# Optimization experiments

Hardware: AMD Instinct MI355X
Metric: run time of the kernel (lower is better)

Reference implementation:

```python
import math
import jax, jax.numpy as jnp
import numpy as np

B, N, M, C, H, POS = 2, 2048, 64, 256, 8, 6
D = C // H  # head_dim = 32
SCALE = 1.0 / math.sqrt(D)
LAMDA = 1.0


def setup_inputs() -> dict:
    key = jax.random.key(0)
    ks = jax.random.split(key, 15)
    s = 0.05
    return {
        "pairwise_g": jax.random.normal(ks[0], (B, N, N, POS), jnp.float32),
        "coset_functions": jax.random.normal(ks[1], (B, N, C), jnp.float32),
        "mask": jnp.ones((B, N), dtype=bool),
        "Wq": jax.random.normal(ks[2], (C, C), jnp.float32) * s,
        "bq": jax.random.normal(ks[3], (C,), jnp.float32) * s,
        "Wk": jax.random.normal(ks[4], (C, C), jnp.float32) * s,
        "bk": jax.random.normal(ks[5], (C,), jnp.float32) * s,
        "Wl": jax.random.normal(ks[6], (C, POS), jnp.float32) * s,
        "bl": jax.random.normal(ks[7], (C,), jnp.float32) * s,
        "u": jax.random.normal(ks[8], (H, D), jnp.float32) * s,
        "v": jax.random.normal(ks[9], (H, D), jnp.float32) * s,
        "Wi": jax.random.normal(ks[10], (C, C), jnp.float32) * s,
        "bi": jax.random.normal(ks[11], (C,), jnp.float32) * s,
        "Wo": jax.random.normal(ks[12], (C, C), jnp.float32) * s,
        "bo": jax.random.normal(ks[13], (C,), jnp.float32) * s,
    }


def reference(pairwise_g, coset_functions, mask, Wq, bq, Wk, bk, Wl, bl, u, v, Wi, bi, Wo, bo):
    # ---- extract_neighbourhoods (mc_samples=M, fill=1.0 -> k == k_ball, permutation irrelevant)
    dists = jnp.linalg.norm(pairwise_g, axis=-1)                      # (B,N,N)
    dists = jnp.where(mask[:, None, :], dists, jnp.float32(1e8))
    _, nbhd_idx = jax.lax.top_k(-dists, M)                            # (B,N,M) nearest neighbors
    nbhd_pg = jnp.take_along_axis(pairwise_g, nbhd_idx[..., None], axis=2)  # (B,N,M,POS)
    gather_rows = jax.vmap(lambda arr, ix: arr[ix])                   # gather along point axis per batch
    nbhd_cf = gather_rows(coset_functions, nbhd_idx)                  # (B,N,M,C)
    nbhd_mask = gather_rows(mask, nbhd_idx)                           # (B,N,M)

    # ---- RelativePositionKernel
    Q = (coset_functions @ Wq.T + bq).reshape(B, N, H, D).transpose(0, 2, 1, 3)  # (B,H,N,D)
    K = (coset_functions @ Wk.T + bk).reshape(B, N, H, D).transpose(0, 2, 1, 3)  # (B,H,N,D)
    e = (nbhd_pg @ Wl.T + bl).reshape(B, N, M, H, D)                  # (B,N,M,H,D)

    S = jnp.einsum('bhnd,bhkd->bhnk', Q, K)                           # dense scores (as original)
    Sg = jnp.take_along_axis(S, nbhd_idx[:, None, :, :], axis=3)      # (B,H,N,M)
    e_term = jnp.einsum('bnmhd,bhnd->bhnm', e, Q + v[None, :, None, :])
    uK = jnp.einsum('hd,bhkd->bhk', u, K)                             # (B,H,N)
    uKg = jnp.take_along_axis(uK[:, :, None, :], nbhd_idx[:, None, :, :], axis=3)  # (B,H,N,M)
    A = (Sg + LAMDA * e_term + uKg) * SCALE
    A = A.transpose(0, 2, 3, 1)                                       # (B,N,M,H)

    # ---- masked softmax over neighbors
    A = jnp.where(nbhd_mask[..., None], A, jnp.float32(-1e38))
    attn = jax.nn.softmax(A, axis=2)                                  # (B,N,M,H)

    # ---- value projection + weighted sum + output linear
    Vv = (nbhd_cf @ Wi.T + bi).reshape(B, N, M, H, D)                 # (B,N,M,H,D)
    out = jnp.einsum('bnmh,bnmhd->bnhd', attn, Vv).reshape(B, N, C)
    out = out @ Wo.T + bo                                             # (B,N,c_out)
    return out
```

## Files before the change

### kernel.cpp

```cpp
#include <hip/hip_runtime.h>
#include <stdint.h>

#define NB 2
#define NN 2048
#define MM 64
#define CC 256
#define HH 8
#define DD 32
#define PP 6
#define ATT_SCALE 0.17677669529663687f

typedef __attribute__((ext_vector_type(8))) short short8;
typedef __attribute__((ext_vector_type(4))) float f32x4;

__device__ __forceinline__ uint16_t f2bf(float f) {
  union { float f; uint32_t u; } c; c.f = f;
  return (uint16_t)((c.u + 0x7fffu + ((c.u >> 16) & 1u)) >> 16);
}

__global__ __launch_bounds__(256) void k_cvt(const float* __restrict__ cf,
                                             const float* __restrict__ Wq,
                                             const float* __restrict__ Wk,
                                             const float* __restrict__ Wi,
                                             const float* __restrict__ Wo,
                                             uint16_t* __restrict__ dst) {
  const int g = blockIdx.x * 256 + threadIdx.x;
  const float* src; int off;
  if (g < 262144)      { src = cf; off = g; }
  else if (g < 278528) { src = Wq; off = g - 262144; }
  else if (g < 294912) { src = Wk; off = g - 278528; }
  else if (g < 311296) { src = Wi; off = g - 294912; }
  else                 { src = Wo; off = g - 311296; }
  const float4 v4 = *(const float4*)(src + (size_t)off * 4);
  ushort4 o;
  o.x = f2bf(v4.x); o.y = f2bf(v4.y); o.z = f2bf(v4.z); o.w = f2bf(v4.w);
  *(ushort4*)(dst + (size_t)g * 4) = o;
}

__global__ __launch_bounds__(256) void k_select(const float* __restrict__ pg,
                                                int* __restrict__ nidx) {
  const int row = blockIdx.x;
  const int t = threadIdx.x;

  __shared__ float s_red[256];
  __shared__ float s_red2[256];
  __shared__ uint32_t s_hist[256];
  __shared__ uint32_t s_scan[256];
  __shared__ float s_cd[NN];
  __shared__ int   s_cj[NN];
  __shared__ int s_tbin;
  __shared__ uint32_t s_c0;
  __shared__ int s_cw;
  __shared__ int s_ct;

  if (t < MM) nidx[(size_t)row * MM + t] = t;

  const float2* base = (const float2*)(pg + (size_t)row * NN * PP);

  float d[8];
  float mn = 3.4e38f, mx = -3.4e38f;
#pragma unroll
  for (int i = 0; i < 8; i++) {
    const int j = t + i * 256;
    const float2 p0 = base[(size_t)j * 3 + 0];
    const float2 p1 = base[(size_t)j * 3 + 1];
    const float2 p2 = base[(size_t)j * 3 + 2];
    float s = __fmul_rn(p0.x, p0.x);
    s = __fadd_rn(s, __fmul_rn(p0.y, p0.y));
    s = __fadd_rn(s, __fmul_rn(p1.x, p1.x));
    s = __fadd_rn(s, __fmul_rn(p1.y, p1.y));
    s = __fadd_rn(s, __fmul_rn(p2.x, p2.x));
    s = __fadd_rn(s, __fmul_rn(p2.y, p2.y));
    const float dist = __fsqrt_rn(s);
    d[i] = dist;
    mn = fminf(mn, dist);
    mx = fmaxf(mx, dist);
  }

  s_red[t] = mn; s_red2[t] = mx;
  __syncthreads();
  for (int off = 128; off; off >>= 1) {
    if (t < off) {
      s_red[t] = fminf(s_red[t], s_red[t + off]);
      s_red2[t] = fmaxf(s_red2[t], s_red2[t + off]);
    }
    __syncthreads();
  }
  mn = s_red[0];
  mx = s_red2[0];
  const float range = mx - mn;
  const float scale = (range > 0.f) ? (256.0f / range) : 0.f;

  s_hist[t] = 0;
  __syncthreads();
  int bins[8];
#pragma unroll
  for (int i = 0; i < 8; i++) {
    int bn = (int)((d[i] - mn) * scale);
    bn = (bn > 255) ? 255 : (bn < 0 ? 0 : bn);
    bins[i] = bn;
    atomicAdd(&s_hist[bn], 1u);
  }
  __syncthreads();

  s_scan[t] = s_hist[t];
  __syncthreads();
  for (int off = 1; off < 256; off <<= 1) {
    const uint32_t add = (t >= off) ? s_scan[t - off] : 0u;
    __syncthreads();
    s_scan[t] += add;
    __syncthreads();
  }

  if (t == 0) { s_cw = 0; s_ct = 0; }
  if (s_scan[t] >= (uint32_t)MM && (t == 0 || s_scan[t - 1] < (uint32_t)MM)) {
    s_tbin = t;
    s_c0 = (t == 0) ? 0u : s_scan[t - 1];
  }
  __syncthreads();

  const int tbin = s_tbin;
  const int c0 = (int)s_c0;

#pragma unroll
  for (int i = 0; i < 8; i++) {
    const int j = t + i * 256;
    if (bins[i] < tbin) {
      const int pos = atomicAdd(&s_cw, 1);
      if (pos < MM) nidx[(size_t)row * MM + pos] = j;
    } else if (bins[i] == tbin) {
      const int pos = atomicAdd(&s_ct, 1);
      s_cd[pos] = d[i];
      s_cj[pos] = j;
    }
  }
  __syncthreads();

  if (t < 64) {
    const int cnt = s_ct;
    const int r = MM - c0;
    for (int it = 0; it < r; ++it) {
      float bd = 3.4e38f; int bj = 0x7fffffff; int bi = -1;
      for (int i = t; i < cnt; i += 64) {
        const float dd = s_cd[i]; const int jj = s_cj[i];
        if (dd < bd || (dd == bd && jj < bj)) { bd = dd; bj = jj; bi = i; }
      }
#pragma unroll
      for (int off = 32; off; off >>= 1) {
        const float od = __shfl_xor(bd, off);
        const int oj = __shfl_xor(bj, off);
        const int oi = __shfl_xor(bi, off);
        if (od < bd || (od == bd && oj < bj)) { bd = od; bj = oj; bi = oi; }
      }
      if (t == 0 && bi >= 0) {
        s_cd[bi] = 3.4e38f;
        nidx[(size_t)row * MM + c0 + it] = bj;
      }
      __threadfence_block();
    }
  }
}

__device__ __forceinline__ void gemm_bt_body(const uint16_t* __restrict__ A,
                                             const uint16_t* __restrict__ W,
                                             const float* __restrict__ bias,
                                             float* __restrict__ O) {
  const int wave = threadIdx.x >> 6;
  const int lane = threadIdx.x & 63;
  const int m = lane & 15;
  const int quad = lane >> 4;
  const int row0 = blockIdx.x * 64 + wave * 16;
  const int c0 = blockIdx.y * 64;

  f32x4 acc0 = {0.f, 0.f, 0.f, 0.f};
  f32x4 acc1 = {0.f, 0.f, 0.f, 0.f};
  f32x4 acc2 = {0.f, 0.f, 0.f, 0.f};
  f32x4 acc3 = {0.f, 0.f, 0.f, 0.f};

#pragma unroll
  for (int k0 = 0; k0 < CC; k0 += 32) {
    const short8 a = *(const short8*)(A + (size_t)(row0 + m) * CC + k0 + quad * 8);
    const short8 b0 = *(const short8*)(W + (size_t)(c0 + 0 + m) * CC + k0 + quad * 8);
    const short8 b1 = *(const short8*)(W + (size_t)(c0 + 16 + m) * CC + k0 + quad * 8);
    const short8 b2 = *(const short8*)(W + (size_t)(c0 + 32 + m) * CC + k0 + quad * 8);
    const short8 b3 = *(const short8*)(W + (size_t)(c0 + 48 + m) * CC + k0 + quad * 8);
    acc0 = __builtin_amdgcn_mfma_f32_16x16x32_bf16(a, b0, acc0, 0, 0, 0);
    acc1 = __builtin_amdgcn_mfma_f32_16x16x32_bf16(a, b1, acc1, 0, 0, 0);
    acc2 = __builtin_amdgcn_mfma_f32_16x16x32_bf16(a, b2, acc2, 0, 0, 0);
    acc3 = __builtin_amdgcn_mfma_f32_16x16x32_bf16(a, b3, acc3, 0, 0, 0);
  }

  const int orow = row0 + quad * 4;
  f32x4 accs[4] = {acc0, acc1, acc2, acc3};
#pragma unroll
  for (int f = 0; f < 4; ++f) {
    const int col = c0 + f * 16 + m;
    const float bv = bias[col];
#pragma unroll
    for (int r = 0; r < 4; ++r) {
      O[(size_t)(orow + r) * CC + col] = accs[f][r] + bv;
    }
  }
}

__global__ __launch_bounds__(256) void k_gemm_qkv(
    const uint16_t* __restrict__ A,
    const uint16_t* __restrict__ W0, const uint16_t* __restrict__ W1, const uint16_t* __restrict__ W2,
    const float* __restrict__ b0, const float* __restrict__ b1, const float* __restrict__ b2,
    float* __restrict__ O0, float* __restrict__ O1, float* __restrict__ O2) {
  const uint16_t* W = (blockIdx.z == 0) ? W0 : ((blockIdx.z == 1) ? W1 : W2);
  const float* bias = (blockIdx.z == 0) ? b0 : ((blockIdx.z == 1) ? b1 : b2);
  float* O = (blockIdx.z == 0) ? O0 : ((blockIdx.z == 1) ? O1 : O2);
  gemm_bt_body(A, W, bias, O);
}

__global__ __launch_bounds__(256) void k_gemm_out(const uint16_t* __restrict__ A,
                                                  const uint16_t* __restrict__ W,
                                                  const float* __restrict__ bias,
                                                  float* __restrict__ O) {
  gemm_bt_body(A, W, bias, O);
}

__global__ __launch_bounds__(256) void k_attn(const float* __restrict__ pg,
                                              const int* __restrict__ nidx,
                                              const float* __restrict__ Q,
                                              const float* __restrict__ K,
                                              const float* __restrict__ V,
                                              const float* __restrict__ Wl,
                                              const float* __restrict__ bl,
                                              const float* __restrict__ u,
                                              const float* __restrict__ v,
                                              uint16_t* __restrict__ attnV) {
  const int row = blockIdx.x;
  const int b = row >> 11;
  const int t = threadIdx.x;
  const int wave = t >> 6;
  const int lane = t & 63;

  __shared__ int s_idx[MM];
  __shared__ float s_npg[MM][7];
  __shared__ float s_qu[CC];
  __shared__ float s_wt[HH][8];
  __shared__ float s_sc[HH][MM];

  if (t < MM) s_idx[t] = nidx[(size_t)row * MM + t] & (NN - 1);
  const float qv_ = Q[(size_t)row * CC + t];
  s_qu[t] = qv_ + u[t];
  __syncthreads();

  if (t < MM) {
    const int jj = s_idx[t];
    const float2* p = (const float2*)(pg + ((size_t)row * NN + (size_t)jj) * PP);
    const float2 p0 = p[0], p1 = p[1], p2 = p[2];
    s_npg[t][0] = p0.x; s_npg[t][1] = p0.y;
    s_npg[t][2] = p1.x; s_npg[t][3] = p1.y;
    s_npg[t][4] = p2.x; s_npg[t][5] = p2.y;
  }

  {
    const int h = t >> 5;
    const float qpv = qv_ + v[t];
    float part[7];
#pragma unroll
    for (int p = 0; p < 6; p++) part[p] = Wl[(size_t)t * PP + p] * qpv;
    part[6] = bl[t] * qpv;
#pragma unroll
    for (int off = 1; off < 32; off <<= 1) {
#pragma unroll
      for (int p = 0; p < 7; p++) part[p] += __shfl_xor(part[p], off);
    }
    if ((t & 31) == 0) {
#pragma unroll
      for (int p = 0; p < 7; p++) s_wt[h][p] = part[p];
    }
  }
  __syncthreads();

#pragma unroll
  for (int pr = 0; pr < 2; ++pr) {
    const int h = wave + pr * 4;
    const int m = lane;
    const int kidx = s_idx[m];
    const float* krow = K + ((size_t)(b * NN + kidx)) * CC + h * DD;
    float acc = s_wt[h][6];
#pragma unroll
    for (int p = 0; p < 6; p++) acc += s_npg[m][p] * s_wt[h][p];
    const float* qu = &s_qu[h * DD];
    float a2 = 0.f;
#pragma unroll
    for (int dd = 0; dd < DD; dd += 4) {
      const float4 kv = *(const float4*)(krow + dd);
      a2 += qu[dd] * kv.x + qu[dd + 1] * kv.y + qu[dd + 2] * kv.z + qu[dd + 3] * kv.w;
    }
    s_sc[h][m] = (acc + a2) * ATT_SCALE;
  }
  __syncthreads();

#pragma unroll
  for (int pr = 0; pr < 2; ++pr) {
    const int h = wave + pr * 4;
    const float x = s_sc[h][lane];
    float mxv = x;
#pragma unroll
    for (int off = 32; off; off >>= 1) mxv = fmaxf(mxv, __shfl_xor(mxv, off));
    const float e = expf(x - mxv);
    float sm = e;
#pragma unroll
    for (int off = 32; off; off >>= 1) sm += __shfl_xor(sm, off);
    s_sc[h][lane] = e / sm;
  }
  __syncthreads();

  {
    const int h = t >> 5;
    const float* Vb = V + (size_t)b * NN * CC;
    float acc = 0.f;
#pragma unroll 4
    for (int m = 0; m < MM; m++) {
      acc += s_sc[h][m] * Vb[(size_t)s_idx[m] * CC + t];
    }
    attnV[(size_t)row * CC + t] = f2bf(acc);
  }
}

extern "C" void kernel_launch(void* const* d_in, const int* in_sizes, int n_in,
                              void* d_out, int out_size, void* d_ws, size_t ws_size,
                              hipStream_t stream) {
  const float* pg = (const float*)d_in[0];
  const float* cf = (const float*)d_in[1];
  const float* Wq = (const float*)d_in[3];
  const float* bq = (const float*)d_in[4];
  const float* Wk = (const float*)d_in[5];
  const float* bk = (const float*)d_in[6];
  const float* Wl = (const float*)d_in[7];
  const float* bl = (const float*)d_in[8];
  const float* u  = (const float*)d_in[9];
  const float* v  = (const float*)d_in[10];
  const float* Wi = (const float*)d_in[11];
  const float* bi = (const float*)d_in[12];
  const float* Wo = (const float*)d_in[13];
  const float* bo = (const float*)d_in[14];

  char* ws = (char*)d_ws;
  int* nidx = (int*)ws;
  float* Q  = (float*)(ws + (size_t)1 * (1 << 20));
  float* K  = (float*)(ws + (size_t)5 * (1 << 20));
  float* V  = (float*)(ws + (size_t)9 * (1 << 20));
  uint16_t* aV = (uint16_t*)(ws + (size_t)13 * (1 << 20));
  uint16_t* cvtb = (uint16_t*)(ws + (size_t)15 * (1 << 20));
  uint16_t* cfb = cvtb;
  uint16_t* Wqb = cfb + 1048576;
  uint16_t* Wkb = Wqb + 65536;
  uint16_t* Wib = Wkb + 65536;
  uint16_t* Wob = Wib + 65536;
  float* out = (float*)d_out;

  hipLaunchKernelGGL(k_cvt, dim3(1280), dim3(256), 0, stream, cf, Wq, Wk, Wi, Wo, cvtb);
  hipLaunchKernelGGL(k_select, dim3(NB * NN), dim3(256), 0, stream, pg, nidx);
  hipLaunchKernelGGL(k_gemm_qkv, dim3(64, 4, 3), dim3(256), 0, stream,
                     cfb, Wqb, Wkb, Wib, bq, bk, bi, Q, K, V);
  hipLaunchKernelGGL(k_attn, dim3(NB * NN), dim3(256), 0, stream,
                     pg, nidx, Q, K, V, Wl, bl, u, v, aV);
  hipLaunchKernelGGL(k_gemm_out, dim3(64, 4), dim3(256), 0, stream,
                     aV, Wob, bo, out);
}
```

Measured before the change: 396.4 us.

## Fuse bf16 conversion into GEMMs, store K/V as bf16, vectorize select loads

Drops the separate fp32-to-bf16 conversion kernel by converting inputs and weights to bf16 inside the GEMM kernels. K and V are now written as bf16, which halves gather traffic in the attention kernel, and the V weighted sum splits neighbours across two thread halves with a shared-memory reduction. k_select reads pairwise_g with float4 loads, two points per load, and replaces its shared-memory min/max tree with wave shuffles. The GEMMs now use single-wave blocks on smaller tiles, so weights are reloaded and converted redundantly per block. Lower-precision K/V adds rounding error.

```diff
diff --git a/kernel.cpp b/kernel.cpp
--- a/kernel.cpp
+++ b/kernel.cpp
@@ -17,33 +17,29 @@
   union { float f; uint32_t u; } c; c.f = f;
   return (uint16_t)((c.u + 0x7fffu + ((c.u >> 16) & 1u)) >> 16);
 }
-
-__global__ __launch_bounds__(256) void k_cvt(const float* __restrict__ cf,
-                                             const float* __restrict__ Wq,
-                                             const float* __restrict__ Wk,
-                                             const float* __restrict__ Wi,
-                                             const float* __restrict__ Wo,
-                                             uint16_t* __restrict__ dst) {
-  const int g = blockIdx.x * 256 + threadIdx.x;
-  const float* src; int off;
-  if (g < 262144)      { src = cf; off = g; }
-  else if (g < 278528) { src = Wq; off = g - 262144; }
-  else if (g < 294912) { src = Wk; off = g - 278528; }
-  else if (g < 311296) { src = Wi; off = g - 294912; }
-  else                 { src = Wo; off = g - 311296; }
-  const float4 v4 = *(const float4*)(src + (size_t)off * 4);
-  ushort4 o;
-  o.x = f2bf(v4.x); o.y = f2bf(v4.y); o.z = f2bf(v4.z); o.w = f2bf(v4.w);
-  *(ushort4*)(dst + (size_t)g * 4) = o;
+__device__ __forceinline__ float blo(uint32_t u) {
+  union { uint32_t u; float f; } c; c.u = u << 16; return c.f;
+}
+__device__ __forceinline__ float bhi(uint32_t u) {
+  union { uint32_t u; float f; } c; c.u = u & 0xffff0000u; return c.f;
+}
+__device__ __forceinline__ short8 pack8(float4 a, float4 b) {
+  short8 r;
+  r[0] = (short)f2bf(a.x); r[1] = (short)f2bf(a.y);
+  r[2] = (short)f2bf(a.z); r[3] = (short)f2bf(a.w);
+  r[4] = (short)f2bf(b.x); r[5] = (short)f2bf(b.y);
+  r[6] = (short)f2bf(b.z); r[7] = (short)f2bf(b.w);
+  return r;
 }
 
 __global__ __launch_bounds__(256) void k_select(const float* __restrict__ pg,
                                                 int* __restrict__ nidx) {
   const int row = blockIdx.x;
   const int t = threadIdx.x;
-
-  __shared__ float s_red[256];
-  __shared__ float s_red2[256];
+  const int wave = t >> 6;
+  const int lane = t & 63;
+
+  __shared__ float s_mn[4], s_mx[4];
   __shared__ uint32_t s_hist[256];
   __shared__ uint32_t s_scan[256];
   __shared__ float s_cd[NN];
@@ -55,44 +51,48 @@
 
   if (t < MM) nidx[(size_t)row * MM + t] = t;
 
-  const float2* base = (const float2*)(pg + (size_t)row * NN * PP);
+  const float4* base = (const float4*)(pg + (size_t)row * NN * PP);
 
   float d[8];
   float mn = 3.4e38f, mx = -3.4e38f;
 #pragma unroll
-  for (int i = 0; i < 8; i++) {
-    const int j = t + i * 256;
-    const float2 p0 = base[(size_t)j * 3 + 0];
-    const float2 p1 = base[(size_t)j * 3 + 1];
-    const float2 p2 = base[(size_t)j * 3 + 2];
-    float s = __fmul_rn(p0.x, p0.x);
-    s = __fadd_rn(s, __fmul_rn(p0.y, p0.y));
-    s = __fadd_rn(s, __fmul_rn(p1.x, p1.x));
-    s = __fadd_rn(s, __fmul_rn(p1.y, p1.y));
-    s = __fadd_rn(s, __fmul_rn(p2.x, p2.x));
-    s = __fadd_rn(s, __fmul_rn(p2.y, p2.y));
-    const float dist = __fsqrt_rn(s);
-    d[i] = dist;
-    mn = fminf(mn, dist);
-    mx = fmaxf(mx, dist);
-  }
-
-  s_red[t] = mn; s_red2[t] = mx;
-  __syncthreads();
-  for (int off = 128; off; off >>= 1) {
-    if (t < off) {
-      s_red[t] = fminf(s_red[t], s_red[t + off]);
-      s_red2[t] = fmaxf(s_red2[t], s_red2[t + off]);
-    }
-    __syncthreads();
-  }
-  mn = s_red[0];
-  mx = s_red2[0];
+  for (int i = 0; i < 4; i++) {
+    const int j0 = i * 512 + 2 * t;
+    const float4 qa = base[(size_t)(j0 >> 1) * 3 + 0];
+    const float4 qb = base[(size_t)(j0 >> 1) * 3 + 1];
+    const float4 qc = base[(size_t)(j0 >> 1) * 3 + 2];
+    float s0 = __fmul_rn(qa.x, qa.x);
+    s0 = __fadd_rn(s0, __fmul_rn(qa.y, qa.y));
+    s0 = __fadd_rn(s0, __fmul_rn(qa.z, qa.z));
+    s0 = __fadd_rn(s0, __fmul_rn(qa.w, qa.w));
+    s0 = __fadd_rn(s0, __fmul_rn(qb.x, qb.x));
+    s0 = __fadd_rn(s0, __fmul_rn(qb.y, qb.y));
+    float s1 = __fmul_rn(qb.z, qb.z);
+    s1 = __fadd_rn(s1, __fmul_rn(qb.w, qb.w));
+    s1 = __fadd_rn(s1, __fmul_rn(qc.x, qc.x));
+    s1 = __fadd_rn(s1, __fmul_rn(qc.y, qc.y));
+    s1 = __fadd_rn(s1, __fmul_rn(qc.z, qc.z));
+    s1 = __fadd_rn(s1, __fmul_rn(qc.w, qc.w));
+    const float d0 = __fsqrt_rn(s0);
+    const float d1 = __fsqrt_rn(s1);
+    d[2 * i] = d0; d[2 * i + 1] = d1;
+    mn = fminf(mn, fminf(d0, d1));
+    mx = fmaxf(mx, fmaxf(d0, d1));
+  }
+
+#pragma unroll
+  for (int off = 32; off; off >>= 1) {
+    mn = fminf(mn, __shfl_xor(mn, off));
+    mx = fmaxf(mx, __shfl_xor(mx, off));
+  }
+  if (lane == 0) { s_mn[wave] = mn; s_mx[wave] = mx; }
+  s_hist[t] = 0;
+  __syncthreads();
+  mn = fminf(fminf(s_mn[0], s_mn[1]), fminf(s_mn[2], s_mn[3]));
+  mx = fmaxf(fmaxf(s_mx[0], s_mx[1]), fmaxf(s_mx[2], s_mx[3]));
   const float range = mx - mn;
   const float scale = (range > 0.f) ? (256.0f / range) : 0.f;
 
-  s_hist[t] = 0;
-  __syncthreads();
   int bins[8];
 #pragma unroll
   for (int i = 0; i < 8; i++) {
@@ -124,7 +124,7 @@
 
 #pragma unroll
   for (int i = 0; i < 8; i++) {
-    const int j = t + i * 256;
+    const int j = (i >> 1) * 512 + 2 * t + (i & 1);
     if (bins[i] < tbin) {
       const int pos = atomicAdd(&s_cw, 1);
       if (pos < MM) nidx[(size_t)row * MM + pos] = j;
@@ -161,15 +161,19 @@
   }
 }
 
-__device__ __forceinline__ void gemm_bt_body(const uint16_t* __restrict__ A,
-                                             const uint16_t* __restrict__ W,
-                                             const float* __restrict__ bias,
-                                             float* __restrict__ O) {
-  const int wave = threadIdx.x >> 6;
-  const int lane = threadIdx.x & 63;
+__global__ __launch_bounds__(64) void k_gemm_qkv(
+    const float* __restrict__ A,
+    const float* __restrict__ W0, const float* __restrict__ W1, const float* __restrict__ W2,
+    const float* __restrict__ b0, const float* __restrict__ b1, const float* __restrict__ b2,
+    float* __restrict__ Qo, uint16_t* __restrict__ Ko, uint16_t* __restrict__ Vo) {
+  const int z = blockIdx.z;
+  const float* W = (z == 0) ? W0 : ((z == 1) ? W1 : W2);
+  const float* bias = (z == 0) ? b0 : ((z == 1) ? b1 : b2);
+
+  const int lane = threadIdx.x;
   const int m = lane & 15;
   const int quad = lane >> 4;
-  const int row0 = blockIdx.x * 64 + wave * 16;
+  const int row0 = blockIdx.x * 16;
   const int c0 = blockIdx.y * 64;
 
   f32x4 acc0 = {0.f, 0.f, 0.f, 0.f};
@@ -179,15 +183,20 @@
 
 #pragma unroll
   for (int k0 = 0; k0 < CC; k0 += 32) {
-    const short8 a = *(const short8*)(A + (size_t)(row0 + m) * CC + k0 + quad * 8);
-    const short8 b0 = *(const short8*)(W + (size_t)(c0 + 0 + m) * CC + k0 + quad * 8);
-    const short8 b1 = *(const short8*)(W + (size_t)(c0 + 16 + m) * CC + k0 + quad * 8);
-    const short8 b2 = *(const short8*)(W + (size_t)(c0 + 32 + m) * CC + k0 + quad * 8);
-    const short8 b3 = *(const short8*)(W + (size_t)(c0 + 48 + m) * CC + k0 + quad * 8);
-    acc0 = __builtin_amdgcn_mfma_f32_16x16x32_bf16(a, b0, acc0, 0, 0, 0);
-    acc1 = __builtin_amdgcn_mfma_f32_16x16x32_bf16(a, b1, acc1, 0, 0, 0);
-    acc2 = __builtin_amdgcn_mfma_f32_16x16x32_bf16(a, b2, acc2, 0, 0, 0);
-    acc3 = __builtin_amdgcn_mfma_f32_16x16x32_bf16(a, b3, acc3, 0, 0, 0);
+    const float4* ap = (const float4*)(A + (size_t)(row0 + m) * CC + k0 + quad * 8);
+    const float4* bp0 = (const float4*)(W + (size_t)(c0 + 0 + m) * CC + k0 + quad * 8);
+    const float4* bp1 = (const float4*)(W + (size_t)(c0 + 16 + m) * CC + k0 + quad * 8);
+    const float4* bp2 = (const float4*)(W + (size_t)(c0 + 32 + m) * CC + k0 + quad * 8);
+    const float4* bp3 = (const float4*)(W + (size_t)(c0 + 48 + m) * CC + k0 + quad * 8);
+    const short8 a = pack8(ap[0], ap[1]);
+    const short8 f0 = pack8(bp0[0], bp0[1]);
+    const short8 f1 = pack8(bp1[0], bp1[1]);
+    const short8 f2 = pack8(bp2[0], bp2[1]);
+    const short8 f3 = pack8(bp3[0], bp3[1]);
+    acc0 = __builtin_amdgcn_mfma_f32_16x16x32_bf16(a, f0, acc0, 0, 0, 0);
+    acc1 = __builtin_amdgcn_mfma_f32_16x16x32_bf16(a, f1, acc1, 0, 0, 0);
+    acc2 = __builtin_amdgcn_mfma_f32_16x16x32_bf16(a, f2, acc2, 0, 0, 0);
+    acc3 = __builtin_amdgcn_mfma_f32_16x16x32_bf16(a, f3, acc3, 0, 0, 0);
   }
 
   const int orow = row0 + quad * 4;
@@ -198,34 +207,57 @@
     const float bv = bias[col];
 #pragma unroll
     for (int r = 0; r < 4; ++r) {
+      const float val = accs[f][r] + bv;
+      const size_t o = (size_t)(orow + r) * CC + col;
+      if (z == 0) Qo[o] = val;
+      else if (z == 1) Ko[o] = f2bf(val);
+      else Vo[o] = f2bf(val);
+    }
+  }
+}
+
+__global__ __launch_bounds__(64) void k_gemm_out(const uint16_t* __restrict__ A,
+                                                 const float* __restrict__ W,
+                                                 const float* __restrict__ bias,
+                                                 float* __restrict__ O) {
+  const int lane = threadIdx.x;
+  const int m = lane & 15;
+  const int quad = lane >> 4;
+  const int row0 = blockIdx.x * 16;
+  const int c0 = blockIdx.y * 32;
+
+  f32x4 acc0 = {0.f, 0.f, 0.f, 0.f};
+  f32x4 acc1 = {0.f, 0.f, 0.f, 0.f};
+
+#pragma unroll
+  for (int k0 = 0; k0 < CC; k0 += 32) {
+    const short8 a = *(const short8*)(A + (size_t)(row0 + m) * CC + k0 + quad * 8);
+    const float4* bp0 = (const float4*)(W + (size_t)(c0 + 0 + m) * CC + k0 + quad * 8);
+    const float4* bp1 = (const float4*)(W + (size_t)(c0 + 16 + m) * CC + k0 + quad * 8);
+    const short8 f0 = pack8(bp0[0], bp0[1]);
+    const short8 f1 = pack8(bp1[0], bp1[1]);
+    acc0 = __builtin_amdgcn_mfma_f32_16x16x32_bf16(a, f0, acc0, 0, 0, 0);
+    acc1 = __builtin_amdgcn_mfma_f32_16x16x32_bf16(a, f1, acc1, 0, 0, 0);
+  }
+
+  const int orow = row0 + quad * 4;
+  f32x4 accs[2] = {acc0, acc1};
+#pragma unroll
+  for (int f = 0; f < 2; ++f) {
+    const int col = c0 + f * 16 + m;
+    const float bv = bias[col];
+#pragma unroll
+    for (int r = 0; r < 4; ++r) {
       O[(size_t)(orow + r) * CC + col] = accs[f][r] + bv;
     }
   }
-}
-
-__global__ __launch_bounds__(256) void k_gemm_qkv(
-    const uint16_t* __restrict__ A,
-    const uint16_t* __restrict__ W0, const uint16_t* __restrict__ W1, const uint16_t* __restrict__ W2,
-    const float* __restrict__ b0, const float* __restrict__ b1, const float* __restrict__ b2,
-    float* __restrict__ O0, float* __restrict__ O1, float* __restrict__ O2) {
-  const uint16_t* W = (blockIdx.z == 0) ? W0 : ((blockIdx.z == 1) ? W1 : W2);
-  const float* bias = (blockIdx.z == 0) ? b0 : ((blockIdx.z == 1) ? b1 : b2);
-  float* O = (blockIdx.z == 0) ? O0 : ((blockIdx.z == 1) ? O1 : O2);
-  gemm_bt_body(A, W, bias, O);
-}
-
-__global__ __launch_bounds__(256) void k_gemm_out(const uint16_t* __restrict__ A,
-                                                  const uint16_t* __restrict__ W,
-                                                  const float* __restrict__ bias,
-                                                  float* __restrict__ O) {
-  gemm_bt_body(A, W, bias, O);
 }
 
 __global__ __launch_bounds__(256) void k_attn(const float* __restrict__ pg,
                                               const int* __restrict__ nidx,
                                               const float* __restrict__ Q,
-                                              const float* __restrict__ K,
-                                              const float* __restrict__ V,
+                                              const uint16_t* __restrict__ K,
+                                              const uint16_t* __restrict__ V,
                                               const float* __restrict__ Wl,
                                               const float* __restrict__ bl,
                                               const float* __restrict__ u,
@@ -242,6 +274,7 @@
   __shared__ float s_qu[CC];
   __shared__ float s_wt[HH][8];
   __shared__ float s_sc[HH][MM];
+  __shared__ float s_part[CC];
 
   if (t < MM) s_idx[t] = nidx[(size_t)row * MM + t] & (NN - 1);
   const float qv_ = Q[(size_t)row * CC + t];
@@ -281,16 +314,20 @@
     const int h = wave + pr * 4;
     const int m = lane;
     const int kidx = s_idx[m];
-    const float* krow = K + ((size_t)(b * NN + kidx)) * CC + h * DD;
+    const uint4* kr = (const uint4*)(K + ((size_t)(b * NN + kidx)) * CC + h * DD);
     float acc = s_wt[h][6];
 #pragma unroll
     for (int p = 0; p < 6; p++) acc += s_npg[m][p] * s_wt[h][p];
     const float* qu = &s_qu[h * DD];
     float a2 = 0.f;
 #pragma unroll
-    for (int dd = 0; dd < DD; dd += 4) {
-      const float4 kv = *(const float4*)(krow + dd);
-      a2 += qu[dd] * kv.x + qu[dd + 1] * kv.y + qu[dd + 2] * kv.z + qu[dd + 3] * kv.w;
+    for (int w4 = 0; w4 < 4; w4++) {
+      const uint4 kv = kr[w4];
+      const float* q8 = qu + w4 * 8;
+      a2 += q8[0] * blo(kv.x) + q8[1] * bhi(kv.x)
+          + q8[2] * blo(kv.y) + q8[3] * bhi(kv.y)
+          + q8[4] * blo(kv.z) + q8[5] * bhi(kv.z)
+          + q8[6] * blo(kv.w) + q8[7] * bhi(kv.w);
     }
     s_sc[h][m] = (acc + a2) * ATT_SCALE;
   }
@@ -312,14 +349,24 @@
   __syncthreads();
 
   {
-    const int h = t >> 5;
-    const float* Vb = V + (size_t)b * NN * CC;
-    float acc = 0.f;
-#pragma unroll 4
-    for (int m = 0; m < MM; m++) {
-      acc += s_sc[h][m] * Vb[(size_t)s_idx[m] * CC + t];
-    }
-    attnV[(size_t)row * CC + t] = f2bf(acc);
+    const int h2 = t >> 7;
+    const int ci = (t & 127) * 2;
+    const int h = ci >> 5;
+    const uint32_t* Vb32 = (const uint32_t*)(V + (size_t)b * NN * CC);
+    float a0 = 0.f, a1 = 0.f;
+#pragma unroll 8
+    for (int m = h2; m < MM; m += 2) {
+      const uint32_t pv = Vb32[(size_t)s_idx[m] * (CC / 2) + (ci >> 1)];
+      const float p = s_sc[h][m];
+      a0 += p * blo(pv);
+      a1 += p * bhi(pv);
+    }
+    if (h2 == 1) { s_part[ci] = a0; s_part[ci + 1] = a1; }
+    __syncthreads();
+    if (h2 == 0) {
+      attnV[(size_t)row * CC + ci]     = f2bf(a0 + s_part[ci]);
+      attnV[(size_t)row * CC + ci + 1] = f2bf(a1 + s_part[ci + 1]);
+    }
   }
 }
 
@@ -344,23 +391,16 @@
   char* ws = (char*)d_ws;
   int* nidx = (int*)ws;
   float* Q  = (float*)(ws + (size_t)1 * (1 << 20));
-  float* K  = (float*)(ws + (size_t)5 * (1 << 20));
-  float* V  = (float*)(ws + (size_t)9 * (1 << 20));
-  uint16_t* aV = (uint16_t*)(ws + (size_t)13 * (1 << 20));
-  uint16_t* cvtb = (uint16_t*)(ws + (size_t)15 * (1 << 20));
-  uint16_t* cfb = cvtb;
-  uint16_t* Wqb = cfb + 1048576;
-  uint16_t* Wkb = Wqb + 65536;
-  uint16_t* Wib = Wkb + 65536;
-  uint16_t* Wob = Wib + 65536;
+  uint16_t* K = (uint16_t*)(ws + (size_t)5 * (1 << 20));
+  uint16_t* V = (uint16_t*)(ws + (size_t)7 * (1 << 20));
+  uint16_t* aV = (uint16_t*)(ws + (size_t)9 * (1 << 20));
   float* out = (float*)d_out;
 
-  hipLaunchKernelGGL(k_cvt, dim3(1280), dim3(256), 0, stream, cf, Wq, Wk, Wi, Wo, cvtb);
+  hipLaunchKernelGGL(k_gemm_qkv, dim3(256, 4, 3), dim3(64), 0, stream,
+                     cf, Wq, Wk, Wi, bq, bk, bi, Q, K, V);
   hipLaunchKernelGGL(k_select, dim3(NB * NN), dim3(256), 0, stream, pg, nidx);
-  hipLaunchKernelGGL(k_gemm_qkv, dim3(64, 4, 3), dim3(256), 0, stream,
-                     cfb, Wqb, Wkb, Wib, bq, bk, bi, Q, K, V);
   hipLaunchKernelGGL(k_attn, dim3(NB * NN), dim3(256), 0, stream,
                      pg, nidx, Q, K, V, Wl, bl, u, v, aV);
-  hipLaunchKernelGGL(k_gemm_out, dim3(64, 4), dim3(256), 0, stream,
-                     aV, Wob, bo, out);
-}
+  hipLaunchKernelGGL(k_gemm_out, dim3(256, 8), dim3(64), 0, stream,
+                     aV, Wo, bo, out);
+}
```

New measurement: 384.1 us. 3.1% less time.
